# Performance work log

Hardware: AMD Instinct MI355X
Metric: run time of the kernel (lower is better)

The kernel has to match this reference:

```python
import jax, jax.numpy as jnp
import numpy as np

N_NODES = 50000
N_EDGES = 800000
NFEAT = 96
NHID = 96
NCLASS = 40


def setup_inputs() -> dict:
    key = jax.random.key(0)
    ks = jax.random.split(key, 8)
    x = jax.random.normal(ks[0], (N_NODES, NFEAT), dtype=jnp.float32)
    edge_index = jax.random.randint(ks[1], (2, N_EDGES), 0, N_NODES, dtype=jnp.int64)
    def glorot(k, shape):
        fan_in = shape[1]
        bound = 1.0 / np.sqrt(fan_in)
        return jax.random.uniform(k, shape, jnp.float32, -bound, bound)
    return {
        'x': x,
        'edge_index': edge_index,
        'W1_l': glorot(ks[2], (NHID, NFEAT)),
        'b1_l': jnp.zeros((NHID,), jnp.float32),
        'W1_r': glorot(ks[3], (NHID, NFEAT)),
        'W2_l': glorot(ks[4], (NCLASS, NHID)),
        'b2_l': jnp.zeros((NCLASS,), jnp.float32),
        'W2_r': glorot(ks[5], (NCLASS, NHID)),
    }


def _sage_conv(x, src, dst, W_l, b_l, W_r):
    # gather neighbor features per edge, scatter-mean onto dst nodes
    msg = x[src]                                   # [E, F]
    agg = jax.ops.segment_sum(msg, dst, num_segments=N_NODES)   # [N, F]
    cnt = jax.ops.segment_sum(jnp.ones((src.shape[0],), x.dtype), dst,
                              num_segments=N_NODES)             # [N]
    agg = agg / jnp.maximum(cnt, 1.0)[:, None]
    # lin_l(agg) + lin_r(x)
    return agg @ W_l.T + b_l + x @ W_r.T


def reference(x, edge_index, W1_l, b1_l, W1_r, W2_l, b2_l, W2_r):
    src, dst = edge_index[0], edge_index[1]
    h = _sage_conv(x, src, dst, W1_l, b1_l, W1_r)
    h = jax.nn.relu(h)  # dropout is identity in eval mode
    h = _sage_conv(h, src, dst, W2_l, b2_l, W2_r)
    return jax.nn.log_softmax(h, axis=1)
```

## Files before the change

### kernel.cpp

```cpp
#include <hip/hip_runtime.h>
#include <hip/hip_fp8.h>
#include <math.h>

#define NCLASS 40
#define BSH    6
#define BSIZE  64
#define MAXB   1024
#define BCAP   2048
#define EPB    4096
#define NCAP   64
#define LSTR   66

typedef __attribute__((ext_vector_type(8))) short short8;
typedef __attribute__((ext_vector_type(4))) float float4v;
typedef __attribute__((ext_vector_type(2))) float float2v;

__device__ __forceinline__ unsigned short f2bf(float f) {
    union { float f; unsigned u; } v; v.f = f;
    unsigned r = v.u + 0x7fffu + ((v.u >> 16) & 1u);
    return (unsigned short)(r >> 16);
}
__device__ __forceinline__ void acc_fp8x4p(unsigned int v, float2v* a2) {
    a2[0] += __builtin_amdgcn_cvt_pk_f32_fp8((int)v, false);
    a2[1] += __builtin_amdgcn_cvt_pk_f32_fp8((int)v, true);
}

__global__ __launch_bounds__(256) void convhist_kernel(const int* __restrict__ ei,
                                                       const float4* __restrict__ x4,
                                                       const float* __restrict__ W1l,
                                                       const float* __restrict__ W1r,
                                                       const float* __restrict__ W2l,
                                                       const float* __restrict__ W2r,
                                                       int* __restrict__ histT,
                                                       unsigned short* __restrict__ xb,
                                                       unsigned char* __restrict__ xq,
                                                       unsigned short* __restrict__ wb1,
                                                       unsigned short* __restrict__ wb2,
                                                       int N, int E, int nbucket,
                                                       int nbin, int xblocks) {
    __shared__ int hcnt[MAXB];
    int tid = threadIdx.x;
    int blk = blockIdx.x;
    if (blk < nbin) {
        for (int t = tid; t < nbucket; t += 256) hcnt[t] = 0;
        __syncthreads();
        int e0 = blk * EPB;
        for (int it = 0; it < EPB / 256; ++it) {
            int e = e0 + it * 256 + tid;
            if (e < E) atomicAdd(&hcnt[ei[E + e] >> BSH], 1);
        }
        __syncthreads();
        for (int t = tid; t < nbucket; t += 256)
            histT[t * nbin + blk] = hcnt[t];
        return;
    }
    if (blk < nbin + xblocks) {
        int idx = (blk - nbin) * 256 + tid;
        if (idx >= N * 24) return;
        int n = idx / 24, q = idx - n * 24;
        float4 v = x4[idx];
        ushort4 o;
        o.x = f2bf(v.x); o.y = f2bf(v.y); o.z = f2bf(v.z); o.w = f2bf(v.w);
        *(ushort4*)(xb + (size_t)n * 96 + q * 4) = o;
        __hip_fp8_e4m3 q0(v.x), q1(v.y), q2(v.z), q3(v.w);
        unsigned int pk = (unsigned)q0.__x | ((unsigned)q1.__x << 8)
                        | ((unsigned)q2.__x << 16) | ((unsigned)q3.__x << 24);
        *(unsigned int*)(xq + (size_t)n * 128 + q * 4) = pk;
        return;
    }
    int t = (blk - nbin - xblocks) * 256 + tid;
    const float* src;
    unsigned short* dst;
    if (t < 36 * 64) {
        int s = t >> 6, lane = t & 63;
        int kc = s / 6, jt = s - kc * 6;
        int j  = jt * 16 + (lane & 15);
        int k2 = kc * 32 + (lane >> 4) * 8;
        src = (k2 < 96) ? (W1l + j * 96 + k2) : (W1r + j * 96 + (k2 - 96));
        dst = wb1 + t * 8;
    } else if (t < 51 * 64) {
        int t2 = t - 36 * 64;
        int s = t2 >> 6, lane = t2 & 63;
        int kc = s / 5, jt = s - kc * 5;
        int j  = jt * 16 + (lane & 15);
        int k2 = kc * 32 + (lane >> 4) * 8;
        src = (j < 40) ? (W2l + j * 96 + k2) : (W2r + (j - 40) * 96 + k2);
        dst = wb2 + t2 * 8;
    } else return;
    ushort4 o0, o1;
    o0.x = f2bf(src[0]); o0.y = f2bf(src[1]); o0.z = f2bf(src[2]); o0.w = f2bf(src[3]);
    o1.x = f2bf(src[4]); o1.y = f2bf(src[5]); o1.z = f2bf(src[6]); o1.w = f2bf(src[7]);
    *(ushort4*)(dst)     = o0;
    *(ushort4*)(dst + 4) = o1;
}

__global__ __launch_bounds__(256) void bsum_kernel(int* __restrict__ histT,
                                                   int* __restrict__ gbh, int nbin) {
    __shared__ int s[256];
    int k = blockIdx.x, tid = threadIdx.x;
    int v = (tid < nbin) ? histT[k * nbin + tid] : 0;
    s[tid] = v;
    __syncthreads();
    for (int off = 1; off < 256; off <<= 1) {
        int o = (tid >= off) ? s[tid - off] : 0;
        __syncthreads();
        s[tid] += o;
        __syncthreads();
    }
    if (tid < nbin) histT[k * nbin + tid] = s[tid] - v;
    if (tid == 255) gbh[k] = s[255];
}

__global__ __launch_bounds__(256) void bin_kernel(const int* __restrict__ ei,
                                                  const int* __restrict__ histT,
                                                  unsigned int* __restrict__ tmp,
                                                  int E, int nbucket, int nbin) {
    __shared__ int lcnt[MAXB];
    __shared__ int lbase[MAXB];
    int tid = threadIdx.x;
    for (int t = tid; t < nbucket; t += 256) {
        lbase[t] = t * BCAP + histT[t * nbin + blockIdx.x];
        lcnt[t]  = 0;
    }
    __syncthreads();
    int e0 = blockIdx.x * EPB;
    for (int it = 0; it < EPB / 256; ++it) {
        int e = e0 + it * 256 + tid;
        if (e < E) {
            int src = ei[e], dst = ei[E + e];
            int b   = dst >> BSH;
            int ofs = atomicAdd(&lcnt[b], 1);
            tmp[lbase[b] + ofs] = (unsigned)src | ((unsigned)(dst & (BSIZE - 1)) << 16);
        }
    }
}

__global__ __launch_bounds__(256) void csr_agg_mm_kernel(const unsigned int* __restrict__ tmp,
                                                         const int* __restrict__ gbh,
                                                         unsigned short* __restrict__ dg,
                                                         unsigned short* __restrict__ col,
                                                         const unsigned char* __restrict__ xq,
                                                         const unsigned short* __restrict__ xb,
                                                         const unsigned short* __restrict__ wb1,
                                                         const float* __restrict__ b1,
                                                         const unsigned short* __restrict__ wb2,
                                                         const float* __restrict__ b2,
                                                         unsigned char* __restrict__ plq,
                                                         float* __restrict__ pr,
                                                         int N) {
    __shared__ int ncnt[BSIZE];
    __shared__ unsigned short lcol[BSIZE * LSTR];
    __shared__ unsigned short sagg[BSIZE * 104];
    int b   = blockIdx.x;
    int tid = threadIdx.x;
    int s0  = b * BCAP;
    int cnt = gbh[b];
    int s1  = s0 + cnt;
    int nodebase = b << BSH;
    if (tid < BSIZE) ncnt[tid] = 0;
    __syncthreads();
    for (int i = s0 + tid; i < s1; i += 256) {
        unsigned int t2 = tmp[i];
        int d = t2 >> 16;
        unsigned short sv = (unsigned short)(t2 & 0xffffu);
        int pos = atomicAdd(&ncnt[d], 1);
        if (pos < NCAP) {
            lcol[d * LSTR + pos] = sv;
            col[((size_t)(nodebase + d) << 6) + pos] = sv;
        }
    }
    __syncthreads();
    if (tid < BSIZE) {
        int degc = ncnt[tid] > NCAP ? NCAP : ncnt[tid];
        ncnt[tid] = degc;
        int node = nodebase + tid;
        if (node < N) dg[node] = (unsigned short)degc;
    }
    __syncthreads();
    for (int item = tid; item < BSIZE * 6; item += 256) {
        int nl = item / 6;
        int q  = item - nl * 6;
        int deg = ncnt[nl];
        const unsigned short* cl = lcol + nl * LSTR;
        float2v a2[8];
        #pragma unroll
        for (int k = 0; k < 8; ++k) a2[k] = float2v{0.f, 0.f};
        int i = 0;
        for (; i + 3 < deg; i += 4) {
            #pragma unroll
            for (int u = 0; u < 4; ++u) {
                int c = (int)cl[i + u];
                uint4 w = *(const uint4*)(xq + (size_t)c * 128 + q * 16);
                acc_fp8x4p(w.x, a2);
                acc_fp8x4p(w.y, a2 + 2);
                acc_fp8x4p(w.z, a2 + 4);
                acc_fp8x4p(w.w, a2 + 6);
            }
        }
        for (; i < deg; ++i) {
            int c = (int)cl[i];
            uint4 w = *(const uint4*)(xq + (size_t)c * 128 + q * 16);
            acc_fp8x4p(w.x, a2);
            acc_fp8x4p(w.y, a2 + 2);
            acc_fp8x4p(w.z, a2 + 4);
            acc_fp8x4p(w.w, a2 + 6);
        }
        float inv = 1.0f / (float)(deg > 1 ? deg : 1);
        ushort4 o0, o1, o2, o3;
        o0.x = f2bf(a2[0][0] * inv); o0.y = f2bf(a2[0][1] * inv);
        o0.z = f2bf(a2[1][0] * inv); o0.w = f2bf(a2[1][1] * inv);
        o1.x = f2bf(a2[2][0] * inv); o1.y = f2bf(a2[2][1] * inv);
        o1.z = f2bf(a2[3][0] * inv); o1.w = f2bf(a2[3][1] * inv);
        o2.x = f2bf(a2[4][0] * inv); o2.y = f2bf(a2[4][1] * inv);
        o2.z = f2bf(a2[5][0] * inv); o2.w = f2bf(a2[5][1] * inv);
        o3.x = f2bf(a2[6][0] * inv); o3.y = f2bf(a2[6][1] * inv);
        o3.z = f2bf(a2[7][0] * inv); o3.w = f2bf(a2[7][1] * inv);
        unsigned short* dst = sagg + nl * 104 + q * 16;
        *(ushort4*)(dst)      = o0;
        *(ushort4*)(dst + 4)  = o1;
        *(ushort4*)(dst + 8)  = o2;
        *(ushort4*)(dst + 12) = o3;
    }
    __syncthreads();

    int wave = tid >> 6, lane = tid & 63;
    int mrow = lane & 15, quad = lane >> 4;
    int lrow = wave * 16 + mrow;
    {
        float4v acc[6] = {};
        const short8* W = (const short8*)wb1;
        #pragma unroll
        for (int kc = 0; kc < 6; ++kc) {
            short8 a0 = (kc < 3)
                ? *(const short8*)&sagg[lrow * 104 + kc * 32 + quad * 8]
                : *(const short8*)(xb + (size_t)(nodebase + lrow) * 96 + (kc - 3) * 32 + quad * 8);
            #pragma unroll
            for (int jt = 0; jt < 6; ++jt) {
                short8 bb = W[(kc * 6 + jt) * 64 + lane];
                acc[jt] = __builtin_amdgcn_mfma_f32_16x16x32_bf16(a0, bb, acc[jt], 0, 0, 0);
            }
        }
        #pragma unroll
        for (int jt = 0; jt < 6; ++jt) {
            int j = jt * 16 + mrow;
            float bj = b1[j];
            #pragma unroll
            for (int r = 0; r < 4; ++r) {
                int nl = wave * 16 + quad * 4 + r;
                sagg[nl * 104 + j] = f2bf(fmaxf(acc[jt][r] + bj, 0.f));
            }
        }
    }
    {
        float4v acc[5] = {};
        const short8* W = (const short8*)wb2;
        #pragma unroll
        for (int kc = 0; kc < 3; ++kc) {
            short8 a0 = *(const short8*)&sagg[lrow * 104 + kc * 32 + quad * 8];
            #pragma unroll
            for (int jt = 0; jt < 5; ++jt) {
                short8 bb = W[(kc * 5 + jt) * 64 + lane];
                acc[jt] = __builtin_amdgcn_mfma_f32_16x16x32_bf16(a0, bb, acc[jt], 0, 0, 0);
            }
        }
        #pragma unroll
        for (int jt = 0; jt < 5; ++jt) {
            int j = jt * 16 + mrow;
            float b2v = (j >= 40) ? b2[j - 40] : 0.f;
            #pragma unroll
            for (int r = 0; r < 4; ++r) {
                int node = nodebase + wave * 16 + quad * 4 + r;
                if (node < N) {
                    float vv = acc[jt][r];
                    if (j < 40) {
                        __hip_fp8_e4m3 qq(vv);
                        plq[(size_t)node * 64 + j] = (unsigned char)qq.__x;
                    } else {
                        pr[(size_t)node * 40 + (j - 40)] = vv + b2v;
                    }
                }
            }
        }
    }
}

__global__ __launch_bounds__(256) void final_kernel(const unsigned char* __restrict__ plq,
                                                    const float* __restrict__ pr,
                                                    const unsigned short* __restrict__ dg,
                                                    const unsigned short* __restrict__ col,
                                                    float* __restrict__ out, int N) {
    __shared__ float red[4][12][40];
    int wave = threadIdx.x >> 6;
    int lane = threadIdx.x & 63;
    int n = blockIdx.x * 4 + wave;
    if (n >= N) return;
    int s   = n << 6;
    int deg = dg[n];
    int e   = s + deg;
    int g = lane / 5;
    int c = lane - g * 5;
    bool gok = (g < 12);
    float2v a2[4];
    #pragma unroll
    for (int k = 0; k < 4; ++k) a2[k] = float2v{0.f, 0.f};
    for (int base = s; base < e; base += 12) {
        int idx = base + g;
        if (gok && idx < e) {
            int cn = col[idx];
            uint2 u = *(const uint2*)(plq + (size_t)cn * 64 + c * 8);
            acc_fp8x4p(u.x, a2);
            acc_fp8x4p(u.y, a2 + 2);
        }
    }
    if (gok) {
        float4 t0, t1;
        t0.x = a2[0][0]; t0.y = a2[0][1]; t0.z = a2[1][0]; t0.w = a2[1][1];
        t1.x = a2[2][0]; t1.y = a2[2][1]; t1.z = a2[3][0]; t1.w = a2[3][1];
        *(float4*)&red[wave][g][c * 8]     = t0;
        *(float4*)&red[wave][g][c * 8 + 4] = t1;
    }
    bool act = (lane < NCLASS);
    float v = -INFINITY;
    if (act) {
        float val = 0.f;
        #pragma unroll
        for (int gg = 0; gg < 12; ++gg) val += red[wave][gg][lane];
        float inv = 1.0f / (float)(deg > 1 ? deg : 1);
        v = val * inv + pr[(size_t)n * 40 + lane];
    }
    float m = v;
    #pragma unroll
    for (int off = 32; off >= 1; off >>= 1) m = fmaxf(m, __shfl_xor(m, off));
    float ex = act ? __expf(v - m) : 0.f;
    float ssum = ex;
    #pragma unroll
    for (int off = 32; off >= 1; off >>= 1) ssum += __shfl_xor(ssum, off);
    if (act) out[(size_t)n * 40 + lane] = v - m - __logf(ssum);
}

extern "C" void kernel_launch(void* const* d_in, const int* in_sizes, int n_in,
                              void* d_out, int out_size, void* d_ws, size_t ws_size,
                              hipStream_t stream) {
    const float* x   = (const float*)d_in[0];
    const int*   ei  = (const int*)  d_in[1];
    const float* W1l = (const float*)d_in[2];
    const float* b1  = (const float*)d_in[3];
    const float* W1r = (const float*)d_in[4];
    const float* W2l = (const float*)d_in[5];
    const float* b2  = (const float*)d_in[6];
    const float* W2r = (const float*)d_in[7];
    float* out = (float*)d_out;

    const int N = in_sizes[0] / 96;
    const int E = in_sizes[1] / 2;
    const int nbucket = (N + BSIZE - 1) >> BSH;
    const int nbin = (E + EPB - 1) / EPB;
    const int NP2  = nbucket * BSIZE;
    const int xblocks = (N * 24 + 255) / 256;

    auto al = [](size_t v) { return (v + 255) & ~(size_t)255; };
    char* ws = (char*)d_ws;
    size_t o = 0;
    int* histT = (int*)(ws + o); o = al(o + (size_t)MAXB * 256 * 4);
    int* gbh   = (int*)(ws + o); o = al(o + (size_t)MAXB * 4);
    unsigned short* dg = (unsigned short*)(ws + o);  o = al(o + (size_t)N * 2);
    unsigned int*   tmp = (unsigned int*)(ws + o);   o = al(o + (size_t)MAXB * BCAP * 4);
    unsigned short* col = (unsigned short*)(ws + o); o = al(o + (size_t)NP2 * NCAP * 2);
    unsigned short* xb  = (unsigned short*)(ws + o); o = al(o + (size_t)NP2 * 96 * 2);
    unsigned char*  xq  = (unsigned char*)(ws + o);  o = al(o + (size_t)NP2 * 128);
    unsigned short* wb1 = (unsigned short*)(ws + o); o = al(o + 36 * 64 * 8 * 2);
    unsigned short* wb2 = (unsigned short*)(ws + o); o = al(o + 15 * 64 * 8 * 2);
    unsigned char*  plq = (unsigned char*)(ws + o);  o = al(o + (size_t)NP2 * 64);
    float*          pr  = (float*)(ws + o);          o = al(o + (size_t)N * 40 * 4);

    convhist_kernel<<<nbin + xblocks + 13, 256, 0, stream>>>(
        ei, (const float4*)x, W1l, W1r, W2l, W2r, histT, xb, xq, wb1, wb2,
        N, E, nbucket, nbin, xblocks);
    bsum_kernel<<<nbucket, 256, 0, stream>>>(histT, gbh, nbin);
    bin_kernel <<<nbin, 256, 0, stream>>>(ei, histT, tmp, E, nbucket, nbin);
    csr_agg_mm_kernel<<<nbucket, 256, 0, stream>>>(
        tmp, gbh, dg, col, xq, xb, wb1, b1, wb2, b2, plq, pr, N);
    final_kernel<<<(N + 3) / 4, 256, 0, stream>>>(plq, pr, dg, col, out, N);
}
```

Before: 152.0 us.

## Fuse histogram, scan and binning into one kernel using global atomic cursors

Replaces the three-kernel edge bucketing pipeline (per-block histogram, per-bucket prefix scan, scatter) with a single pass. Each block counts its edges per bucket in shared memory, records each edge's local offset, reserves space in the bucket through a global atomicAdd on a cursor array, then scatters. This removes two kernel launches and the histT round-trip through global memory, at the cost of a memset and nondeterministic edge order within buckets.

```diff
diff --git a/kernel.cpp b/kernel.cpp
--- a/kernel.cpp
+++ b/kernel.cpp
@@ -25,33 +25,53 @@
     a2[1] += __builtin_amdgcn_cvt_pk_f32_fp8((int)v, true);
 }
 
-__global__ __launch_bounds__(256) void convhist_kernel(const int* __restrict__ ei,
-                                                       const float4* __restrict__ x4,
-                                                       const float* __restrict__ W1l,
-                                                       const float* __restrict__ W1r,
-                                                       const float* __restrict__ W2l,
-                                                       const float* __restrict__ W2r,
-                                                       int* __restrict__ histT,
-                                                       unsigned short* __restrict__ xb,
-                                                       unsigned char* __restrict__ xq,
-                                                       unsigned short* __restrict__ wb1,
-                                                       unsigned short* __restrict__ wb2,
-                                                       int N, int E, int nbucket,
-                                                       int nbin, int xblocks) {
-    __shared__ int hcnt[MAXB];
+__global__ __launch_bounds__(256) void convbin_kernel(const int* __restrict__ ei,
+                                                      const float4* __restrict__ x4,
+                                                      const float* __restrict__ W1l,
+                                                      const float* __restrict__ W1r,
+                                                      const float* __restrict__ W2l,
+                                                      const float* __restrict__ W2r,
+                                                      int* __restrict__ gcur,
+                                                      unsigned int* __restrict__ tmp,
+                                                      unsigned short* __restrict__ xb,
+                                                      unsigned char* __restrict__ xq,
+                                                      unsigned short* __restrict__ wb1,
+                                                      unsigned short* __restrict__ wb2,
+                                                      int N, int E, int nbucket,
+                                                      int nbin, int xblocks) {
     int tid = threadIdx.x;
     int blk = blockIdx.x;
     if (blk < nbin) {
-        for (int t = tid; t < nbucket; t += 256) hcnt[t] = 0;
+        __shared__ int lcnt[MAXB];
+        __shared__ int lbase[MAXB];
+        __shared__ unsigned short lofs[EPB];
+        for (int t = tid; t < nbucket; t += 256) lcnt[t] = 0;
         __syncthreads();
         int e0 = blk * EPB;
         for (int it = 0; it < EPB / 256; ++it) {
-            int e = e0 + it * 256 + tid;
-            if (e < E) atomicAdd(&hcnt[ei[E + e] >> BSH], 1);
+            int li = it * 256 + tid;
+            int e  = e0 + li;
+            if (e < E) {
+                int b = ei[E + e] >> BSH;
+                lofs[li] = (unsigned short)atomicAdd(&lcnt[b], 1);
+            }
         }
         __syncthreads();
-        for (int t = tid; t < nbucket; t += 256)
-            histT[t * nbin + blk] = hcnt[t];
+        for (int t = tid; t < nbucket; t += 256) {
+            int c = lcnt[t];
+            lbase[t] = t * BCAP + (c ? atomicAdd(&gcur[t], c) : 0);
+        }
+        __syncthreads();
+        for (int it = 0; it < EPB / 256; ++it) {
+            int li = it * 256 + tid;
+            int e  = e0 + li;
+            if (e < E) {
+                int src = ei[e], dst = ei[E + e];
+                int b   = dst >> BSH;
+                tmp[lbase[b] + lofs[li]] =
+                    (unsigned)src | ((unsigned)(dst & (BSIZE - 1)) << 16);
+            }
+        }
         return;
     }
     if (blk < nbin + xblocks) {
@@ -92,47 +112,6 @@
     o1.x = f2bf(src[4]); o1.y = f2bf(src[5]); o1.z = f2bf(src[6]); o1.w = f2bf(src[7]);
     *(ushort4*)(dst)     = o0;
     *(ushort4*)(dst + 4) = o1;
-}
-
-__global__ __launch_bounds__(256) void bsum_kernel(int* __restrict__ histT,
-                                                   int* __restrict__ gbh, int nbin) {
-    __shared__ int s[256];
-    int k = blockIdx.x, tid = threadIdx.x;
-    int v = (tid < nbin) ? histT[k * nbin + tid] : 0;
-    s[tid] = v;
-    __syncthreads();
-    for (int off = 1; off < 256; off <<= 1) {
-        int o = (tid >= off) ? s[tid - off] : 0;
-        __syncthreads();
-        s[tid] += o;
-        __syncthreads();
-    }
-    if (tid < nbin) histT[k * nbin + tid] = s[tid] - v;
-    if (tid == 255) gbh[k] = s[255];
-}
-
-__global__ __launch_bounds__(256) void bin_kernel(const int* __restrict__ ei,
-                                                  const int* __restrict__ histT,
-                                                  unsigned int* __restrict__ tmp,
-                                                  int E, int nbucket, int nbin) {
-    __shared__ int lcnt[MAXB];
-    __shared__ int lbase[MAXB];
-    int tid = threadIdx.x;
-    for (int t = tid; t < nbucket; t += 256) {
-        lbase[t] = t * BCAP + histT[t * nbin + blockIdx.x];
-        lcnt[t]  = 0;
-    }
-    __syncthreads();
-    int e0 = blockIdx.x * EPB;
-    for (int it = 0; it < EPB / 256; ++it) {
-        int e = e0 + it * 256 + tid;
-        if (e < E) {
-            int src = ei[e], dst = ei[E + e];
-            int b   = dst >> BSH;
-            int ofs = atomicAdd(&lcnt[b], 1);
-            tmp[lbase[b] + ofs] = (unsigned)src | ((unsigned)(dst & (BSIZE - 1)) << 16);
-        }
-    }
 }
 
 __global__ __launch_bounds__(256) void csr_agg_mm_kernel(const unsigned int* __restrict__ tmp,
@@ -361,8 +340,7 @@
     auto al = [](size_t v) { return (v + 255) & ~(size_t)255; };
     char* ws = (char*)d_ws;
     size_t o = 0;
-    int* histT = (int*)(ws + o); o = al(o + (size_t)MAXB * 256 * 4);
-    int* gbh   = (int*)(ws + o); o = al(o + (size_t)MAXB * 4);
+    int* gcur = (int*)(ws + o);                      o = al(o + (size_t)MAXB * 4);
     unsigned short* dg = (unsigned short*)(ws + o);  o = al(o + (size_t)N * 2);
     unsigned int*   tmp = (unsigned int*)(ws + o);   o = al(o + (size_t)MAXB * BCAP * 4);
     unsigned short* col = (unsigned short*)(ws + o); o = al(o + (size_t)NP2 * NCAP * 2);
@@ -373,12 +351,11 @@
     unsigned char*  plq = (unsigned char*)(ws + o);  o = al(o + (size_t)NP2 * 64);
     float*          pr  = (float*)(ws + o);          o = al(o + (size_t)N * 40 * 4);
 
-    convhist_kernel<<<nbin + xblocks + 13, 256, 0, stream>>>(
-        ei, (const float4*)x, W1l, W1r, W2l, W2r, histT, xb, xq, wb1, wb2,
+    hipMemsetAsync(gcur, 0, (size_t)MAXB * 4, stream);
+    convbin_kernel<<<nbin + xblocks + 13, 256, 0, stream>>>(
+        ei, (const float4*)x, W1l, W1r, W2l, W2r, gcur, tmp, xb, xq, wb1, wb2,
         N, E, nbucket, nbin, xblocks);
-    bsum_kernel<<<nbucket, 256, 0, stream>>>(histT, gbh, nbin);
-    bin_kernel <<<nbin, 256, 0, stream>>>(ei, histT, tmp, E, nbucket, nbin);
     csr_agg_mm_kernel<<<nbucket, 256, 0, stream>>>(
-        tmp, gbh, dg, col, xq, xb, wb1, b1, wb2, b2, plq, pr, N);
+        tmp, gcur, dg, col, xq, xb, wb1, b1, wb2, b2, plq, pr, N);
     final_kernel<<<(N + 3) / 4, 256, 0, stream>>>(plq, pr, dg, col, out, N);
 }
```

Result: no change. 150.4 us (-1.0%).
